# Kernel tuning notes

Measured on AMD Instinct MI355X. Metric: run time of the kernel, lower is better.

## Reference

```python
import jax, jax.numpy as jnp
import numpy as np

HIDDEN = 1024
BATCH = 32
SEQ = 2048


def setup_inputs() -> dict:
    key = jax.random.key(0)
    k1, k2, k3, k4, k5 = jax.random.split(key, 5)
    current_hidden = jax.random.normal(k1, (BATCH, HIDDEN), dtype=jnp.float32)
    past_hidden = jax.random.normal(k2, (BATCH, SEQ, HIDDEN), dtype=jnp.float32)
    # nn.Linear(2H, H): weight (H, 2H), bias (H)
    s = 1.0 / np.sqrt(2 * HIDDEN)
    W_proj = jax.random.uniform(k3, (HIDDEN, 2 * HIDDEN), jnp.float32, -s, s)
    b_proj = jax.random.uniform(k4, (HIDDEN,), jnp.float32, -s, s)
    # nn.Linear(H, 1, bias=False): weight (1, H) -> store as (H,)
    s2 = 1.0 / np.sqrt(HIDDEN)
    w_score = jax.random.uniform(k5, (HIDDEN,), jnp.float32, -s2, s2)
    return {
        "current_hidden": current_hidden,
        "past_hidden": past_hidden,
        "W_proj": W_proj,
        "b_proj": b_proj,
        "w_score": w_score,
    }


def reference(current_hidden, past_hidden, W_proj, b_proj, w_score):
    # concat(past, current) @ W_proj.T == past @ Wp.T + current @ Wc.T (linear split)
    H = W_proj.shape[0]
    Wp = W_proj[:, :H]   # acts on past_hidden
    Wc = W_proj[:, H:]   # acts on current_hidden
    # energy: (B, S, H)
    energy = jnp.tanh(
        jnp.einsum("bsd,hd->bsh", past_hidden, Wp)
        + (jnp.einsum("bd,hd->bh", current_hidden, Wc) + b_proj)[:, None, :]
    )
    scores = jnp.einsum("bsh,h->bs", energy, w_score)  # (B, S)
    attn_weights = jax.nn.softmax(scores, axis=-1)
    attended = jnp.einsum("bs,bsd->bd", attn_weights, past_hidden)  # (B, H)
    return attended, attn_weights
```

## Files before the change

kernel.cpp:

```cpp
#include <hip/hip_runtime.h>
#include <hip/hip_bf16.h>

#define HID 1024
#define BATCH 32
#define SEQ 2048
#define MROWS (BATCH*SEQ)

typedef __bf16 bf16x8 __attribute__((ext_vector_type(8)));
typedef float f32x4 __attribute__((ext_vector_type(4)));

__device__ __forceinline__ unsigned short f2bf(float f) {
  unsigned int x = __float_as_uint(f);
  x += 0x7FFFu + ((x >> 16) & 1u);
  return (unsigned short)(x >> 16);
}

__global__ __launch_bounds__(256) void prep_kernel(
    const float* __restrict__ cur, const float* __restrict__ Wproj,
    const float* __restrict__ bproj, unsigned short* __restrict__ Bbf,
    float* __restrict__ c_ws)
{
  int h = blockIdx.x, t = threadIdx.x;
  float4 v = ((const float4*)(Wproj + (long)h * 2048))[t];
  ushort4 u; u.x = f2bf(v.x); u.y = f2bf(v.y); u.z = f2bf(v.z); u.w = f2bf(v.w);
  ((ushort4*)(Bbf + (long)h * 1024))[t] = u;

  __shared__ float wc[HID];
  float4 w4 = ((const float4*)(Wproj + (long)h * 2048 + 1024))[t];
  ((float4*)wc)[t] = w4;
  __syncthreads();

  int wv = t >> 6, l = t & 63;
  float bp = bproj[h];
  for (int i = 0; i < 8; ++i) {
    int b = wv * 8 + i;
    const float* cb = cur + b * HID;
    float s = 0.f;
    #pragma unroll
    for (int j = 0; j < 16; ++j) { int d = l + j * 64; s += cb[d] * wc[d]; }
    #pragma unroll
    for (int m = 1; m < 64; m <<= 1) s += __shfl_xor(s, m, 64);
    if (l == 0) c_ws[b * HID + h] = s + bp;
  }
}

#define BM 128
#define BN 128
#define BK 64

__global__ __launch_bounds__(256) void score_gemm(
    const float* __restrict__ past, const unsigned short* __restrict__ Bbf,
    const float* __restrict__ c_ws, const float* __restrict__ wsc,
    float* __restrict__ scores)
{
  __shared__ unsigned short As[BM * BK];
  __shared__ unsigned short Bs[BN * BK];

  int bid = blockIdx.x;
  int wg = (bid & 7) * 512 + (bid >> 3);
  int mt = wg >> 3, nt = wg & 7;
  long row0 = (long)mt * BM;
  int n0 = nt * BN;
  int b = mt >> 4;

  int t = threadIdx.x;
  int w = t >> 6, lane = t & 63;
  int wr = w >> 1, wcn = w & 1;
  int la = lane & 15, lb = lane >> 4;

  f32x4 acc[4][4] = {};

  for (int kt = 0; kt < HID / BK; ++kt) {
    int k0 = kt * BK;
    float4 av[8];
    #pragma unroll
    for (int i = 0; i < 8; ++i) {
      int c = t + 256 * i;
      int r = c >> 4, fc = c & 15;
      av[i] = ((const float4*)(past + (row0 + r) * 1024 + k0))[fc];
    }
    __syncthreads();
    #pragma unroll
    for (int i = 0; i < 8; ++i) {
      int c = t + 256 * i;
      int r = c >> 4, fc = c & 15;
      int off = (r * 128 + fc * 8) ^ ((r & 7) << 4);
      ushort4 uu; uu.x = f2bf(av[i].x); uu.y = f2bf(av[i].y);
      uu.z = f2bf(av[i].z); uu.w = f2bf(av[i].w);
      *(ushort4*)((char*)As + off) = uu;
    }
    #pragma unroll
    for (int i = 0; i < 4; ++i) {
      int o = (t + 256 * i) * 16;
      int uoff = o ^ (((o >> 7) & 7) << 4);
      int n = uoff >> 7, inb = uoff & 127;
      const unsigned short* src = Bbf + (long)(n0 + n) * 1024 + k0 + (inb >> 1);
      __builtin_amdgcn_global_load_lds(
          (const __attribute__((address_space(1))) void*)src,
          (__attribute__((address_space(3))) void*)((char*)Bs + o), 16, 0, 0);
    }
    __syncthreads();
    #pragma unroll
    for (int kk = 0; kk < 2; ++kk) {
      bf16x8 af[4], bfv[4];
      #pragma unroll
      for (int m = 0; m < 4; ++m) {
        int r = wr * 64 + m * 16 + la;
        int off = (r * 128 + kk * 64 + lb * 16) ^ ((r & 7) << 4);
        af[m] = *(const bf16x8*)((const char*)As + off);
      }
      #pragma unroll
      for (int n = 0; n < 4; ++n) {
        int r = wcn * 64 + n * 16 + la;
        int off = (r * 128 + kk * 64 + lb * 16) ^ ((r & 7) << 4);
        bfv[n] = *(const bf16x8*)((const char*)Bs + off);
      }
      #pragma unroll
      for (int m = 0; m < 4; ++m)
        #pragma unroll
        for (int n = 0; n < 4; ++n)
          acc[m][n] = __builtin_amdgcn_mfma_f32_16x16x32_bf16(
              af[m], bfv[n], acc[m][n], 0, 0, 0);
    }
  }

  const float* crow = c_ws + b * HID;
  float ch[4], wv4[4];
  #pragma unroll
  for (int n = 0; n < 4; ++n) {
    int h = n0 + wcn * 64 + n * 16 + la;
    ch[n] = crow[h];
    wv4[n] = wsc[h];
  }
  #pragma unroll
  for (int m = 0; m < 4; ++m) {
    #pragma unroll
    for (int j = 0; j < 4; ++j) {
      float rs = 0.f;
      #pragma unroll
      for (int n = 0; n < 4; ++n)
        rs += wv4[n] * tanhf(acc[m][n][j] + ch[n]);
      rs += __shfl_xor(rs, 1, 64);
      rs += __shfl_xor(rs, 2, 64);
      rs += __shfl_xor(rs, 4, 64);
      rs += __shfl_xor(rs, 8, 64);
      if (la == 0) {
        long grow = row0 + wr * 64 + m * 16 + lb * 4 + j;
        atomicAdd(scores + grow, rs);
      }
    }
  }
}

__global__ __launch_bounds__(256) void softmax_kernel(float* __restrict__ sc)
{
  int b = blockIdx.x, t = threadIdx.x;
  float* row = sc + (long)b * SEQ;
  float v[8]; float mx = -1e30f;
  #pragma unroll
  for (int j = 0; j < 8; ++j) { v[j] = row[t + j * 256]; mx = fmaxf(mx, v[j]); }
  #pragma unroll
  for (int m = 1; m < 64; m <<= 1) mx = fmaxf(mx, __shfl_xor(mx, m, 64));
  __shared__ float rmax[4], rsum[4];
  if ((t & 63) == 0) rmax[t >> 6] = mx;
  __syncthreads();
  mx = fmaxf(fmaxf(rmax[0], rmax[1]), fmaxf(rmax[2], rmax[3]));
  float s = 0.f;
  #pragma unroll
  for (int j = 0; j < 8; ++j) { v[j] = expf(v[j] - mx); s += v[j]; }
  #pragma unroll
  for (int m = 1; m < 64; m <<= 1) s += __shfl_xor(s, m, 64);
  if ((t & 63) == 0) rsum[t >> 6] = s;
  __syncthreads();
  float inv = 1.f / (rsum[0] + rsum[1] + rsum[2] + rsum[3]);
  #pragma unroll
  for (int j = 0; j < 8; ++j) row[t + j * 256] = v[j] * inv;
}

__global__ __launch_bounds__(256) void attend_partial(
    const float* __restrict__ past, const float* __restrict__ attn,
    float* __restrict__ partial)
{
  int blk = blockIdx.x;
  int b = blk >> 4, scn = blk & 15;
  int t = threadIdx.x;
  int s0 = scn * 128;
  __shared__ float aw[128];
  if (t < 128) aw[t] = attn[(long)b * SEQ + s0 + t];
  __syncthreads();
  const float4* pp = (const float4*)(past + ((long)(b * SEQ + s0)) * HID);
  float ax = 0.f, ay = 0.f, az = 0.f, awv = 0.f;
  #pragma unroll 4
  for (int s = 0; s < 128; ++s) {
    float wgt = aw[s];
    float4 v = pp[s * 256 + t];
    ax += wgt * v.x; ay += wgt * v.y; az += wgt * v.z; awv += wgt * v.w;
  }
  float4 o; o.x = ax; o.y = ay; o.z = az; o.w = awv;
  ((float4*)(partial + (long)blk * HID))[t] = o;
}

__global__ __launch_bounds__(256) void attend_reduce(
    const float* __restrict__ partial, float* __restrict__ out)
{
  int blk = blockIdx.x;
  int b = blk >> 2, d = (blk & 3) * 256 + threadIdx.x;
  float s = 0.f;
  #pragma unroll
  for (int sc = 0; sc < 16; ++sc) s += partial[(long)(b * 16 + sc) * HID + d];
  out[(long)b * HID + d] = s;
}

extern "C" void kernel_launch(void* const* d_in, const int* in_sizes, int n_in,
                              void* d_out, int out_size, void* d_ws, size_t ws_size,
                              hipStream_t stream)
{
  const float* cur   = (const float*)d_in[0];
  const float* past  = (const float*)d_in[1];
  const float* Wproj = (const float*)d_in[2];
  const float* bproj = (const float*)d_in[3];
  const float* wsc   = (const float*)d_in[4];

  float* out      = (float*)d_out;
  float* attended = out;
  float* scores   = out + 32768;

  char* ws = (char*)d_ws;
  float*          c_ws    = (float*)ws;
  unsigned short* Bbf     = (unsigned short*)(ws + (128 << 10));
  float*          partial = (float*)(ws + (128 << 10) + (2 << 20));

  hipMemsetAsync(scores, 0, (size_t)BATCH * SEQ * sizeof(float), stream);
  prep_kernel<<<1024, 256, 0, stream>>>(cur, Wproj, bproj, Bbf, c_ws);
  score_gemm<<<4096, 256, 0, stream>>>(past, Bbf, c_ws, wsc, scores);
  softmax_kernel<<<BATCH, 256, 0, stream>>>(scores);
  attend_partial<<<512, 256, 0, stream>>>(past, scores, partial);
  attend_reduce<<<128, 256, 0, stream>>>(partial, attended);
}
```

Baseline: 659.5 us.

## Pre-convert past_hidden to bf16 and load GEMM tiles directly into LDS

Adds a separate pass that converts past_hidden to bf16 in a large workspace buffer. A new GEMM variant then streams both A and B tiles into LDS with global_load_lds, with no register staging and no XOR swizzle. The attend stage is split into 64 chunks per batch instead of 16. The conversion adds an extra full read of past plus a 128MB write and read-back, and dropping the swizzle risks LDS bank conflicts; the fast path runs only if the workspace is large enough.

Measured after the change: 737.7 us. 11.9% more time.

```diff
diff --git a/kernel.cpp b/kernel.cpp
--- a/kernel.cpp
+++ b/kernel.cpp
@@ -13,6 +13,21 @@
   unsigned int x = __float_as_uint(f);
   x += 0x7FFFu + ((x >> 16) & 1u);
   return (unsigned short)(x >> 16);
+}
+
+__global__ __launch_bounds__(256) void convert_past(
+    const float* __restrict__ past, unsigned short* __restrict__ Abf)
+{
+  const long n8 = (long)MROWS * HID / 8;
+  const long stride = (long)gridDim.x * 256;
+  for (long i = (long)blockIdx.x * 256 + threadIdx.x; i < n8; i += stride) {
+    float4 a = ((const float4*)past)[2 * i];
+    float4 b = ((const float4*)past)[2 * i + 1];
+    bf16x8 o;
+    o[0] = (__bf16)a.x; o[1] = (__bf16)a.y; o[2] = (__bf16)a.z; o[3] = (__bf16)a.w;
+    o[4] = (__bf16)b.x; o[5] = (__bf16)b.y; o[6] = (__bf16)b.z; o[7] = (__bf16)b.w;
+    ((bf16x8*)Abf)[i] = o;
+  }
 }
 
 __global__ __launch_bounds__(256) void prep_kernel(
@@ -48,8 +63,8 @@
 #define BN 128
 #define BK 64
 
-__global__ __launch_bounds__(256) void score_gemm(
-    const float* __restrict__ past, const unsigned short* __restrict__ Bbf,
+__global__ __launch_bounds__(256) void score_gemm_bf(
+    const unsigned short* __restrict__ Abf, const unsigned short* __restrict__ Bbf,
     const float* __restrict__ c_ws, const float* __restrict__ wsc,
     float* __restrict__ scores)
 {
@@ -72,32 +87,19 @@
 
   for (int kt = 0; kt < HID / BK; ++kt) {
     int k0 = kt * BK;
-    float4 av[8];
-    #pragma unroll
-    for (int i = 0; i < 8; ++i) {
+    __syncthreads();
+    #pragma unroll
+    for (int i = 0; i < 4; ++i) {
       int c = t + 256 * i;
-      int r = c >> 4, fc = c & 15;
-      av[i] = ((const float4*)(past + (row0 + r) * 1024 + k0))[fc];
-    }
-    __syncthreads();
-    #pragma unroll
-    for (int i = 0; i < 8; ++i) {
-      int c = t + 256 * i;
-      int r = c >> 4, fc = c & 15;
-      int off = (r * 128 + fc * 8) ^ ((r & 7) << 4);
-      ushort4 uu; uu.x = f2bf(av[i].x); uu.y = f2bf(av[i].y);
-      uu.z = f2bf(av[i].z); uu.w = f2bf(av[i].w);
-      *(ushort4*)((char*)As + off) = uu;
-    }
-    #pragma unroll
-    for (int i = 0; i < 4; ++i) {
-      int o = (t + 256 * i) * 16;
-      int uoff = o ^ (((o >> 7) & 7) << 4);
-      int n = uoff >> 7, inb = uoff & 127;
-      const unsigned short* src = Bbf + (long)(n0 + n) * 1024 + k0 + (inb >> 1);
+      int r = c >> 3, fc = (c & 7) * 8;
+      const unsigned short* srcA = Abf + (row0 + r) * 1024 + k0 + fc;
       __builtin_amdgcn_global_load_lds(
-          (const __attribute__((address_space(1))) void*)src,
-          (__attribute__((address_space(3))) void*)((char*)Bs + o), 16, 0, 0);
+          (const __attribute__((address_space(1))) void*)srcA,
+          (__attribute__((address_space(3))) void*)((char*)As + c * 16), 16, 0, 0);
+      const unsigned short* srcB = Bbf + (long)(n0 + r) * 1024 + k0 + fc;
+      __builtin_amdgcn_global_load_lds(
+          (const __attribute__((address_space(1))) void*)srcB,
+          (__attribute__((address_space(3))) void*)((char*)Bs + c * 16), 16, 0, 0);
     }
     __syncthreads();
     #pragma unroll
@@ -106,14 +108,12 @@
       #pragma unroll
       for (int m = 0; m < 4; ++m) {
         int r = wr * 64 + m * 16 + la;
-        int off = (r * 128 + kk * 64 + lb * 16) ^ ((r & 7) << 4);
-        af[m] = *(const bf16x8*)((const char*)As + off);
+        af[m] = *(const bf16x8*)((const char*)As + r * 128 + kk * 64 + lb * 16);
       }
       #pragma unroll
       for (int n = 0; n < 4; ++n) {
         int r = wcn * 64 + n * 16 + la;
-        int off = (r * 128 + kk * 64 + lb * 16) ^ ((r & 7) << 4);
-        bfv[n] = *(const bf16x8*)((const char*)Bs + off);
+        bfv[n] = *(const bf16x8*)((const char*)Bs + r * 128 + kk * 64 + lb * 16);
       }
       #pragma unroll
       for (int m = 0; m < 4; ++m)
@@ -152,6 +152,110 @@
   }
 }
 
+__global__ __launch_bounds__(256) void score_gemm(
+    const float* __restrict__ past, const unsigned short* __restrict__ Bbf,
+    const float* __restrict__ c_ws, const float* __restrict__ wsc,
+    float* __restrict__ scores)
+{
+  __shared__ unsigned short As[BM * BK];
+  __shared__ unsigned short Bs[BN * BK];
+
+  int bid = blockIdx.x;
+  int wg = (bid & 7) * 512 + (bid >> 3);
+  int mt = wg >> 3, nt = wg & 7;
+  long row0 = (long)mt * BM;
+  int n0 = nt * BN;
+  int b = mt >> 4;
+
+  int t = threadIdx.x;
+  int w = t >> 6, lane = t & 63;
+  int wr = w >> 1, wcn = w & 1;
+  int la = lane & 15, lb = lane >> 4;
+
+  f32x4 acc[4][4] = {};
+
+  for (int kt = 0; kt < HID / BK; ++kt) {
+    int k0 = kt * BK;
+    float4 av[8];
+    #pragma unroll
+    for (int i = 0; i < 8; ++i) {
+      int c = t + 256 * i;
+      int r = c >> 4, fc = c & 15;
+      av[i] = ((const float4*)(past + (row0 + r) * 1024 + k0))[fc];
+    }
+    __syncthreads();
+    #pragma unroll
+    for (int i = 0; i < 8; ++i) {
+      int c = t + 256 * i;
+      int r = c >> 4, fc = c & 15;
+      int off = (r * 128 + fc * 8) ^ ((r & 7) << 4);
+      ushort4 uu; uu.x = f2bf(av[i].x); uu.y = f2bf(av[i].y);
+      uu.z = f2bf(av[i].z); uu.w = f2bf(av[i].w);
+      *(ushort4*)((char*)As + off) = uu;
+    }
+    #pragma unroll
+    for (int i = 0; i < 4; ++i) {
+      int o = (t + 256 * i) * 16;
+      int uoff = o ^ (((o >> 7) & 7) << 4);
+      int n = uoff >> 7, inb = uoff & 127;
+      const unsigned short* src = Bbf + (long)(n0 + n) * 1024 + k0 + (inb >> 1);
+      __builtin_amdgcn_global_load_lds(
+          (const __attribute__((address_space(1))) void*)src,
+          (__attribute__((address_space(3))) void*)((char*)Bs + o), 16, 0, 0);
+    }
+    __syncthreads();
+    #pragma unroll
+    for (int kk = 0; kk < 2; ++kk) {
+      bf16x8 af[4], bfv[4];
+      #pragma unroll
+      for (int m = 0; m < 4; ++m) {
+        int r = wr * 64 + m * 16 + la;
+        int off = (r * 128 + kk * 64 + lb * 16) ^ ((r & 7) << 4);
+        af[m] = *(const bf16x8*)((const char*)As + off);
+      }
+      #pragma unroll
+      for (int n = 0; n < 4; ++n) {
+        int r = wcn * 64 + n * 16 + la;
+        int off = (r * 128 + kk * 64 + lb * 16) ^ ((r & 7) << 4);
+        bfv[n] = *(const bf16x8*)((const char*)Bs + off);
+      }
+      #pragma unroll
+      for (int m = 0; m < 4; ++m)
+        #pragma unroll
+        for (int n = 0; n < 4; ++n)
+          acc[m][n] = __builtin_amdgcn_mfma_f32_16x16x32_bf16(
+              af[m], bfv[n], acc[m][n], 0, 0, 0);
+    }
+  }
+
+  const float* crow = c_ws + b * HID;
+  float ch[4], wv4[4];
+  #pragma unroll
+  for (int n = 0; n < 4; ++n) {
+    int h = n0 + wcn * 64 + n * 16 + la;
+    ch[n] = crow[h];
+    wv4[n] = wsc[h];
+  }
+  #pragma unroll
+  for (int m = 0; m < 4; ++m) {
+    #pragma unroll
+    for (int j = 0; j < 4; ++j) {
+      float rs = 0.f;
+      #pragma unroll
+      for (int n = 0; n < 4; ++n)
+        rs += wv4[n] * tanhf(acc[m][n][j] + ch[n]);
+      rs += __shfl_xor(rs, 1, 64);
+      rs += __shfl_xor(rs, 2, 64);
+      rs += __shfl_xor(rs, 4, 64);
+      rs += __shfl_xor(rs, 8, 64);
+      if (la == 0) {
+        long grow = row0 + wr * 64 + m * 16 + lb * 4 + j;
+        atomicAdd(scores + grow, rs);
+      }
+    }
+  }
+}
+
 __global__ __launch_bounds__(256) void softmax_kernel(float* __restrict__ sc)
 {
   int b = blockIdx.x, t = threadIdx.x;
@@ -179,19 +283,20 @@
 
 __global__ __launch_bounds__(256) void attend_partial(
     const float* __restrict__ past, const float* __restrict__ attn,
-    float* __restrict__ partial)
+    float* __restrict__ partial, int cshift)
 {
   int blk = blockIdx.x;
-  int b = blk >> 4, scn = blk & 15;
+  int b = blk >> cshift, scn = blk & ((1 << cshift) - 1);
+  int rows = SEQ >> cshift;
   int t = threadIdx.x;
-  int s0 = scn * 128;
+  int s0 = scn * rows;
   __shared__ float aw[128];
-  if (t < 128) aw[t] = attn[(long)b * SEQ + s0 + t];
+  if (t < rows) aw[t] = attn[(long)b * SEQ + s0 + t];
   __syncthreads();
   const float4* pp = (const float4*)(past + ((long)(b * SEQ + s0)) * HID);
   float ax = 0.f, ay = 0.f, az = 0.f, awv = 0.f;
   #pragma unroll 4
-  for (int s = 0; s < 128; ++s) {
+  for (int s = 0; s < rows; ++s) {
     float wgt = aw[s];
     float4 v = pp[s * 256 + t];
     ax += wgt * v.x; ay += wgt * v.y; az += wgt * v.z; awv += wgt * v.w;
@@ -201,13 +306,13 @@
 }
 
 __global__ __launch_bounds__(256) void attend_reduce(
-    const float* __restrict__ partial, float* __restrict__ out)
+    const float* __restrict__ partial, float* __restrict__ out, int nchunks)
 {
   int blk = blockIdx.x;
   int b = blk >> 2, d = (blk & 3) * 256 + threadIdx.x;
   float s = 0.f;
-  #pragma unroll
-  for (int sc = 0; sc < 16; ++sc) s += partial[(long)(b * 16 + sc) * HID + d];
+  for (int sc = 0; sc < nchunks; ++sc)
+    s += partial[(long)(b * nchunks + sc) * HID + d];
   out[(long)b * HID + d] = s;
 }
 
@@ -229,11 +334,25 @@
   float*          c_ws    = (float*)ws;
   unsigned short* Bbf     = (unsigned short*)(ws + (128 << 10));
   float*          partial = (float*)(ws + (128 << 10) + (2 << 20));
+  unsigned short* Abf     = (unsigned short*)(ws + (128 << 10) + (10 << 20));
+
+  const size_t NEED_FAST = (size_t)(128 << 10) + (10 << 20) + ((size_t)128 << 20);
+  const bool fast = ws_size >= NEED_FAST;
 
   hipMemsetAsync(scores, 0, (size_t)BATCH * SEQ * sizeof(float), stream);
   prep_kernel<<<1024, 256, 0, stream>>>(cur, Wproj, bproj, Bbf, c_ws);
-  score_gemm<<<4096, 256, 0, stream>>>(past, Bbf, c_ws, wsc, scores);
+  if (fast) {
+    convert_past<<<2048, 256, 0, stream>>>(past, Abf);
+    score_gemm_bf<<<4096, 256, 0, stream>>>(Abf, Bbf, c_ws, wsc, scores);
+  } else {
+    score_gemm<<<4096, 256, 0, stream>>>(past, Bbf, c_ws, wsc, scores);
+  }
   softmax_kernel<<<BATCH, 256, 0, stream>>>(scores);
-  attend_partial<<<512, 256, 0, stream>>>(past, scores, partial);
-  attend_reduce<<<128, 256, 0, stream>>>(partial, attended);
-}
+  if (fast) {
+    attend_partial<<<32 * 64, 256, 0, stream>>>(past, scores, partial, 6);
+    attend_reduce<<<128, 256, 0, stream>>>(partial, attended, 64);
+  } else {
+    attend_partial<<<32 * 16, 256, 0, stream>>>(past, scores, partial, 4);
+    attend_reduce<<<128, 256, 0, stream>>>(partial, attended, 16);
+  }
+}
```

## Double-buffer score GEMM tiles and split attend over more blocks

Applied to the files above, without the earlier changes.

The score GEMM now keeps two LDS buffers for the A and B tiles. It prefetches the next K-tile's fp32 A values into registers and DMAs the next B tile while the current tile's MFMAs run, so only one barrier is needed per iteration. Address computation is hoisted out of the loop, the bf16 conversion uses native casts, and a launch bound of two blocks per SM is added. The attend_partial kernel splits the sequence into 64 chunks instead of 16, giving 2048 blocks for better bandwidth occupancy, at the cost of a larger partial buffer and more reduce work. The design also relies on the workspace being large enough for the bigger partial buffer, and doubling LDS to 64KB per block may limit occupancy.

Measured after the change: 698.4 us. +5.9%, slower.

```diff
diff --git a/kernel.cpp b/kernel.cpp
--- a/kernel.cpp
+++ b/kernel.cpp
@@ -4,7 +4,6 @@
 #define HID 1024
 #define BATCH 32
 #define SEQ 2048
-#define MROWS (BATCH*SEQ)
 
 typedef __bf16 bf16x8 __attribute__((ext_vector_type(8)));
 typedef float f32x4 __attribute__((ext_vector_type(4)));
@@ -48,13 +47,13 @@
 #define BN 128
 #define BK 64
 
-__global__ __launch_bounds__(256) void score_gemm(
+__global__ __launch_bounds__(256, 2) void score_gemm(
     const float* __restrict__ past, const unsigned short* __restrict__ Bbf,
     const float* __restrict__ c_ws, const float* __restrict__ wsc,
     float* __restrict__ scores)
 {
-  __shared__ unsigned short As[BM * BK];
-  __shared__ unsigned short Bs[BN * BK];
+  __shared__ unsigned short As[2][BM * BK];
+  __shared__ unsigned short Bs[2][BN * BK];
 
   int bid = blockIdx.x;
   int wg = (bid & 7) * 512 + (bid >> 3);
@@ -68,38 +67,53 @@
   int wr = w >> 1, wcn = w & 1;
   int la = lane & 15, lb = lane >> 4;
 
+  const float* aptr[4];
+  const unsigned short* bptr[4];
+  int awoff[4], bdoff[4];
+  #pragma unroll
+  for (int i = 0; i < 4; ++i) {
+    int c = t + 256 * i;
+    int r = c >> 3, q = c & 7;
+    aptr[i] = past + (row0 + r) * 1024 + q * 8;
+    awoff[i] = (r * 128 + q * 16) ^ ((r & 7) << 4);
+    int o = c * 16;
+    int uoff = o ^ (((o >> 7) & 7) << 4);
+    int n = uoff >> 7, inb = uoff & 127;
+    bptr[i] = Bbf + (long)(n0 + n) * 1024 + (inb >> 1);
+    bdoff[i] = o;
+  }
+
   f32x4 acc[4][4] = {};
-
-  for (int kt = 0; kt < HID / BK; ++kt) {
-    int k0 = kt * BK;
-    float4 av[8];
-    #pragma unroll
-    for (int i = 0; i < 8; ++i) {
-      int c = t + 256 * i;
-      int r = c >> 4, fc = c & 15;
-      av[i] = ((const float4*)(past + (row0 + r) * 1024 + k0))[fc];
-    }
-    __syncthreads();
-    #pragma unroll
-    for (int i = 0; i < 8; ++i) {
-      int c = t + 256 * i;
-      int r = c >> 4, fc = c & 15;
-      int off = (r * 128 + fc * 8) ^ ((r & 7) << 4);
-      ushort4 uu; uu.x = f2bf(av[i].x); uu.y = f2bf(av[i].y);
-      uu.z = f2bf(av[i].z); uu.w = f2bf(av[i].w);
-      *(ushort4*)((char*)As + off) = uu;
-    }
+  float4 areg[4][2];
+
+  auto LOADA = [&](int kt) {
     #pragma unroll
     for (int i = 0; i < 4; ++i) {
-      int o = (t + 256 * i) * 16;
-      int uoff = o ^ (((o >> 7) & 7) << 4);
-      int n = uoff >> 7, inb = uoff & 127;
-      const unsigned short* src = Bbf + (long)(n0 + n) * 1024 + k0 + (inb >> 1);
+      const float* p = aptr[i] + kt * BK;
+      areg[i][0] = *(const float4*)p;
+      areg[i][1] = *(const float4*)(p + 4);
+    }
+  };
+  auto DMAB = [&](int kt, int buf) {
+    #pragma unroll
+    for (int i = 0; i < 4; ++i)
       __builtin_amdgcn_global_load_lds(
-          (const __attribute__((address_space(1))) void*)src,
-          (__attribute__((address_space(3))) void*)((char*)Bs + o), 16, 0, 0);
-    }
-    __syncthreads();
+          (const __attribute__((address_space(1))) void*)(bptr[i] + kt * BK),
+          (__attribute__((address_space(3))) void*)((char*)Bs[buf] + bdoff[i]),
+          16, 0, 0);
+  };
+  auto WRITEA = [&](int buf) {
+    #pragma unroll
+    for (int i = 0; i < 4; ++i) {
+      bf16x8 o;
+      o[0] = (__bf16)areg[i][0].x; o[1] = (__bf16)areg[i][0].y;
+      o[2] = (__bf16)areg[i][0].z; o[3] = (__bf16)areg[i][0].w;
+      o[4] = (__bf16)areg[i][1].x; o[5] = (__bf16)areg[i][1].y;
+      o[6] = (__bf16)areg[i][1].z; o[7] = (__bf16)areg[i][1].w;
+      *(bf16x8*)((char*)As[buf] + awoff[i]) = o;
+    }
+  };
+  auto COMPUTE = [&](int buf) {
     #pragma unroll
     for (int kk = 0; kk < 2; ++kk) {
       bf16x8 af[4], bfv[4];
@@ -107,13 +121,13 @@
       for (int m = 0; m < 4; ++m) {
         int r = wr * 64 + m * 16 + la;
         int off = (r * 128 + kk * 64 + lb * 16) ^ ((r & 7) << 4);
-        af[m] = *(const bf16x8*)((const char*)As + off);
+        af[m] = *(const bf16x8*)((const char*)As[buf] + off);
       }
       #pragma unroll
       for (int n = 0; n < 4; ++n) {
         int r = wcn * 64 + n * 16 + la;
         int off = (r * 128 + kk * 64 + lb * 16) ^ ((r & 7) << 4);
-        bfv[n] = *(const bf16x8*)((const char*)Bs + off);
+        bfv[n] = *(const bf16x8*)((const char*)Bs[buf] + off);
       }
       #pragma unroll
       for (int m = 0; m < 4; ++m)
@@ -122,7 +136,21 @@
           acc[m][n] = __builtin_amdgcn_mfma_f32_16x16x32_bf16(
               af[m], bfv[n], acc[m][n], 0, 0, 0);
     }
-  }
+  };
+
+  LOADA(0); DMAB(0, 0); WRITEA(0);
+  __syncthreads();
+
+  #pragma unroll 2
+  for (int kt = 0; kt < 15; ++kt) {
+    int cur = kt & 1;
+    LOADA(kt + 1);
+    DMAB(kt + 1, cur ^ 1);
+    COMPUTE(cur);
+    WRITEA(cur ^ 1);
+    __syncthreads();
+  }
+  COMPUTE(1);
 
   const float* crow = c_ws + b * HID;
   float ch[4], wv4[4];
@@ -182,16 +210,16 @@
     float* __restrict__ partial)
 {
   int blk = blockIdx.x;
-  int b = blk >> 4, scn = blk & 15;
+  int b = blk >> 6, scn = blk & 63;
   int t = threadIdx.x;
-  int s0 = scn * 128;
-  __shared__ float aw[128];
-  if (t < 128) aw[t] = attn[(long)b * SEQ + s0 + t];
+  int s0 = scn * 32;
+  __shared__ float aw[32];
+  if (t < 32) aw[t] = attn[(long)b * SEQ + s0 + t];
   __syncthreads();
   const float4* pp = (const float4*)(past + ((long)(b * SEQ + s0)) * HID);
   float ax = 0.f, ay = 0.f, az = 0.f, awv = 0.f;
   #pragma unroll 4
-  for (int s = 0; s < 128; ++s) {
+  for (int s = 0; s < 32; ++s) {
     float wgt = aw[s];
     float4 v = pp[s * 256 + t];
     ax += wgt * v.x; ay += wgt * v.y; az += wgt * v.z; awv += wgt * v.w;
@@ -207,7 +235,8 @@
   int b = blk >> 2, d = (blk & 3) * 256 + threadIdx.x;
   float s = 0.f;
   #pragma unroll
-  for (int sc = 0; sc < 16; ++sc) s += partial[(long)(b * 16 + sc) * HID + d];
+  for (int sc = 0; sc < 64; ++sc)
+    s += partial[(long)(b * 64 + sc) * HID + d];
   out[(long)b * HID + d] = s;
 }
 
@@ -234,6 +263,6 @@
   prep_kernel<<<1024, 256, 0, stream>>>(cur, Wproj, bproj, Bbf, c_ws);
   score_gemm<<<4096, 256, 0, stream>>>(past, Bbf, c_ws, wsc, scores);
   softmax_kernel<<<BATCH, 256, 0, stream>>>(scores);
-  attend_partial<<<512, 256, 0, stream>>>(past, scores, partial);
+  attend_partial<<<32 * 64, 256, 0, stream>>>(past, scores, partial);
   attend_reduce<<<128, 256, 0, stream>>>(partial, attended);
 }
```
